# Kernel tuning notes

Measured on AMD Instinct MI355X. Metric: run time of the kernel, lower is better.

The kernel has to match this reference:

```python
import jax, jax.numpy as jnp
import numpy as np

N, K, D = 16384, 2048, 512

def setup_inputs() -> dict:
    key = jax.random.key(0)
    kx, kmu, kstd = jax.random.split(key, 3)
    x = jax.random.normal(kx, (N, D), dtype=jnp.float32)
    mu = jax.random.normal(kmu, (K, D), dtype=jnp.float32)
    std = jax.random.uniform(kstd, (K, D), dtype=jnp.float32)  # positive so log(sum(std)) is defined
    return {"x": x, "mu": mu, "std": std}

def reference(x, mu, std):
    x_sq = jnp.sum(x * x, axis=1)                      # [N]
    mu_sq = jnp.sum(mu * mu, axis=1)                   # [K]
    sqdist = x_sq[:, None] - 2.0 * (x @ mu.T) + mu_sq[None, :]  # [N, K]
    denom = 2.0 * jnp.sum(std * std, axis=1) + 1e-8    # [K]
    log_std_sum = jnp.log(jnp.sum(std, axis=1))        # [K]
    half_log_2pi = 0.5 * jnp.log(jnp.asarray(2.0 * np.pi, dtype=x.dtype))
    return -sqdist / denom[None, :] - log_std_sum[None, :] - half_log_2pi
```

## Files before the change

### kernel.cpp

```cpp
#include <hip/hip_runtime.h>
#include <hip/hip_bf16.h>
#include <stdint.h>

#define NN 16384
#define KK 2048
#define DD 512

typedef __bf16 bf16x8 __attribute__((ext_vector_type(8)));
typedef float f32x4 __attribute__((ext_vector_type(4)));
typedef unsigned short ushort_t;
typedef ushort_t us8 __attribute__((ext_vector_type(8)));

#define AS1(p) ((const __attribute__((address_space(1))) void*)(p))
#define AS3(p) ((__attribute__((address_space(3))) void*)(p))

__device__ inline ushort_t f2bf(float f) {
  uint32_t u = __float_as_uint(f);
  u += 0x7fffu + ((u >> 16) & 1u);
  return (ushort_t)(u >> 16);
}

__global__ __launch_bounds__(256) void prep_x(const float* __restrict__ x,
                                              ushort_t* __restrict__ xb,
                                              float* __restrict__ x_sq) {
  const int wave = threadIdx.x >> 6;
  const int lane = threadIdx.x & 63;
  const int row = blockIdx.x * 4 + wave;
  const float* xr = x + (size_t)row * DD + lane * 8;
  float4 v0 = *reinterpret_cast<const float4*>(xr);
  float4 v1 = *reinterpret_cast<const float4*>(xr + 4);
  float s = v0.x*v0.x + v0.y*v0.y + v0.z*v0.z + v0.w*v0.w
          + v1.x*v1.x + v1.y*v1.y + v1.z*v1.z + v1.w*v1.w;
  us8 o;
  o[0]=f2bf(v0.x); o[1]=f2bf(v0.y); o[2]=f2bf(v0.z); o[3]=f2bf(v0.w);
  o[4]=f2bf(v1.x); o[5]=f2bf(v1.y); o[6]=f2bf(v1.z); o[7]=f2bf(v1.w);
  *reinterpret_cast<us8*>(xb + (size_t)row * DD + lane * 8) = o;
  #pragma unroll
  for (int off = 32; off; off >>= 1) s += __shfl_xor(s, off, 64);
  if (lane == 0) x_sq[row] = s;
}

__global__ __launch_bounds__(256) void prep_mu(const float* __restrict__ mu,
                                               const float* __restrict__ sd,
                                               ushort_t* __restrict__ mub,
                                               float* __restrict__ inv_denom,
                                               float* __restrict__ beta) {
  const int wave = threadIdx.x >> 6;
  const int lane = threadIdx.x & 63;
  const int row = blockIdx.x * 4 + wave;
  const float* mr = mu + (size_t)row * DD + lane * 8;
  float4 v0 = *reinterpret_cast<const float4*>(mr);
  float4 v1 = *reinterpret_cast<const float4*>(mr + 4);
  float musq = v0.x*v0.x + v0.y*v0.y + v0.z*v0.z + v0.w*v0.w
             + v1.x*v1.x + v1.y*v1.y + v1.z*v1.z + v1.w*v1.w;
  us8 o;
  o[0]=f2bf(v0.x); o[1]=f2bf(v0.y); o[2]=f2bf(v0.z); o[3]=f2bf(v0.w);
  o[4]=f2bf(v1.x); o[5]=f2bf(v1.y); o[6]=f2bf(v1.z); o[7]=f2bf(v1.w);
  *reinterpret_cast<us8*>(mub + (size_t)row * DD + lane * 8) = o;

  const float* sr = sd + (size_t)row * DD + lane * 8;
  float4 s0 = *reinterpret_cast<const float4*>(sr);
  float4 s1 = *reinterpret_cast<const float4*>(sr + 4);
  float ssum = s0.x + s0.y + s0.z + s0.w + s1.x + s1.y + s1.z + s1.w;
  float ssq  = s0.x*s0.x + s0.y*s0.y + s0.z*s0.z + s0.w*s0.w
             + s1.x*s1.x + s1.y*s1.y + s1.z*s1.z + s1.w*s1.w;
  #pragma unroll
  for (int off = 32; off; off >>= 1) {
    musq += __shfl_xor(musq, off, 64);
    ssum += __shfl_xor(ssum, off, 64);
    ssq  += __shfl_xor(ssq,  off, 64);
  }
  if (lane == 0) {
    float idn = 1.0f / (2.0f * ssq + 1e-8f);
    inv_denom[row] = idn;
    beta[row] = musq * idn + logf(ssum) + 0.91893853320467274f;
  }
}

__global__ __launch_bounds__(256) void gemm_eval(const ushort_t* __restrict__ xb,
                                                 const ushort_t* __restrict__ mub,
                                                 const float* __restrict__ x_sq,
                                                 const float* __restrict__ inv_denom,
                                                 const float* __restrict__ beta,
                                                 float* __restrict__ out) {
  __shared__ __align__(16) ushort_t As[128 * 32];
  __shared__ __align__(16) ushort_t Bs[128 * 32];

  const int t = threadIdx.x;
  const int lane = t & 63;
  const int w = t >> 6;
  const int wrow = w >> 1;
  const int wcol = w & 1;

  const int bm = blockIdx.x >> 4;
  const int bn = blockIdx.x & 15;
  const int brow = bm * 128;
  const int bcol = bn * 128;

  f32x4 acc[4][4];
  #pragma unroll
  for (int m = 0; m < 4; ++m)
    #pragma unroll
    for (int c = 0; c < 4; ++c)
      acc[m][c] = (f32x4){0.f, 0.f, 0.f, 0.f};

  const int c0 = t;
  const int c1 = t + 256;

  const int rl = lane & 15;
  const int slot = lane >> 4;

  for (int kt = 0; kt < DD / 32; ++kt) {
    const int kb = kt * 32;
    {
      const ushort_t* g0 = xb + (size_t)(brow + (c0 >> 2)) * DD + kb + (c0 & 3) * 8;
      __builtin_amdgcn_global_load_lds(AS1(g0), AS3(As + c0 * 8), 16, 0, 0);
      const ushort_t* g1 = xb + (size_t)(brow + (c1 >> 2)) * DD + kb + (c1 & 3) * 8;
      __builtin_amdgcn_global_load_lds(AS1(g1), AS3(As + c1 * 8), 16, 0, 0);
      const ushort_t* h0 = mub + (size_t)(bcol + (c0 >> 2)) * DD + kb + (c0 & 3) * 8;
      __builtin_amdgcn_global_load_lds(AS1(h0), AS3(Bs + c0 * 8), 16, 0, 0);
      const ushort_t* h1 = mub + (size_t)(bcol + (c1 >> 2)) * DD + kb + (c1 & 3) * 8;
      __builtin_amdgcn_global_load_lds(AS1(h1), AS3(Bs + c1 * 8), 16, 0, 0);
    }
    __syncthreads();

    const bf16x8* A8 = reinterpret_cast<const bf16x8*>(As);
    const bf16x8* B8 = reinterpret_cast<const bf16x8*>(Bs);
    bf16x8 af[4], bfr[4];
    #pragma unroll
    for (int m = 0; m < 4; ++m)
      af[m] = A8[(wrow * 64 + m * 16 + rl) * 4 + slot];
    #pragma unroll
    for (int c = 0; c < 4; ++c)
      bfr[c] = B8[(wcol * 64 + c * 16 + rl) * 4 + slot];

    #pragma unroll
    for (int m = 0; m < 4; ++m)
      #pragma unroll
      for (int c = 0; c < 4; ++c)
        acc[m][c] = __builtin_amdgcn_mfma_f32_16x16x32_bf16(af[m], bfr[c], acc[m][c], 0, 0, 0);

    __syncthreads();
  }

  const int rh = lane >> 4;
  float inv[4], bet[4];
  #pragma unroll
  for (int c = 0; c < 4; ++c) {
    int k = bcol + wcol * 64 + c * 16 + rl;
    inv[c] = inv_denom[k];
    bet[c] = beta[k];
  }
  #pragma unroll
  for (int m = 0; m < 4; ++m) {
    #pragma unroll
    for (int r = 0; r < 4; ++r) {
      int n = brow + wrow * 64 + m * 16 + rh * 4 + r;
      float xs = x_sq[n];
      size_t base = (size_t)n * KK + bcol + wcol * 64;
      #pragma unroll
      for (int c = 0; c < 4; ++c) {
        out[base + c * 16 + rl] = (2.0f * acc[m][c][r] - xs) * inv[c] - bet[c];
      }
    }
  }
}

extern "C" void kernel_launch(void* const* d_in, const int* in_sizes, int n_in,
                              void* d_out, int out_size, void* d_ws, size_t ws_size,
                              hipStream_t stream) {
  const float* x   = (const float*)d_in[0];
  const float* mu  = (const float*)d_in[1];
  const float* sd  = (const float*)d_in[2];
  float* out = (float*)d_out;

  char* ws = (char*)d_ws;
  ushort_t* xb        = (ushort_t*)(ws);
  ushort_t* mub       = (ushort_t*)(ws + 16777216);
  float*    x_sq      = (float*)(ws + 18874368);
  float*    inv_denom = (float*)(ws + 18939904);
  float*    beta      = (float*)(ws + 18948096);

  prep_x<<<NN / 4, 256, 0, stream>>>(x, xb, x_sq);
  prep_mu<<<KK / 4, 256, 0, stream>>>(mu, sd, mub, inv_denom, beta);
  gemm_eval<<<(NN / 128) * (KK / 128), 256, 0, stream>>>(xb, mub, x_sq, inv_denom, beta, out);
}
```

Baseline: 202.3 us.

## Retile GEMM to 256x256 blocks with MFMA-ready layout and double-buffered LDS

The prep kernels now write the bf16 copies of x and mu in a pre-tiled, fragment-ordered layout, so each K-tile is one contiguous 32 KB chunk that can be copied straight into LDS and read with conflict-free per-lane loads. The GEMM grows to 256x256 tiles with 512 threads and 64-deep K steps. It double-buffers LDS so the next tile's global-to-LDS copy overlaps the MFMAs, and it adds block-index swizzling and s_setprio around the MFMA bursts. Together these aim to raise data reuse and cut both the LDS bank conflicts and the per-iteration barrier stalls. The cost is 128 KB of LDS per block, more accumulator registers, a fixed-shape layout, and hand-placed barriers and waitcnts that must stay correct.

```diff
diff --git a/kernel.cpp b/kernel.cpp
--- a/kernel.cpp
+++ b/kernel.cpp
@@ -14,11 +14,16 @@
 #define AS1(p) ((const __attribute__((address_space(1))) void*)(p))
 #define AS3(p) ((__attribute__((address_space(3))) void*)(p))
 
+#define FENCE() asm volatile("" ::: "memory")
+#define SBAR()  do { FENCE(); __builtin_amdgcn_s_barrier(); FENCE(); } while (0)
+#define WAITVM0() asm volatile("s_waitcnt vmcnt(0)" ::: "memory")
+
 __device__ inline ushort_t f2bf(float f) {
   uint32_t u = __float_as_uint(f);
   u += 0x7fffu + ((u >> 16) & 1u);
   return (ushort_t)(u >> 16);
 }
+
 
 __global__ __launch_bounds__(256) void prep_x(const float* __restrict__ x,
                                               ushort_t* __restrict__ xb,
@@ -34,9 +39,14 @@
   us8 o;
   o[0]=f2bf(v0.x); o[1]=f2bf(v0.y); o[2]=f2bf(v0.z); o[3]=f2bf(v0.w);
   o[4]=f2bf(v1.x); o[5]=f2bf(v1.y); o[6]=f2bf(v1.z); o[7]=f2bf(v1.w);
-  *reinterpret_cast<us8*>(xb + (size_t)row * DD + lane * 8) = o;
-  #pragma unroll
-  for (int off = 32; off; off >>= 1) s += __shfl_xor(s, off, 64);
+
+  const int br = row >> 8, m = (row >> 4) & 15, r = row & 15;
+  const int kt = lane >> 3, cc2 = lane & 7, ks = cc2 >> 2, slot = cc2 & 3;
+  size_t off = (size_t)(br * 8 + kt) * 16384 + (m * 2 + ks) * 512 + slot * 128 + r * 8;
+  *reinterpret_cast<us8*>(xb + off) = o;
+
+  #pragma unroll
+  for (int offs = 32; offs; offs >>= 1) s += __shfl_xor(s, offs, 64);
   if (lane == 0) x_sq[row] = s;
 }
 
@@ -56,7 +66,11 @@
   us8 o;
   o[0]=f2bf(v0.x); o[1]=f2bf(v0.y); o[2]=f2bf(v0.z); o[3]=f2bf(v0.w);
   o[4]=f2bf(v1.x); o[5]=f2bf(v1.y); o[6]=f2bf(v1.z); o[7]=f2bf(v1.w);
-  *reinterpret_cast<us8*>(mub + (size_t)row * DD + lane * 8) = o;
+
+  const int bc = row >> 8, cB = (row >> 4) & 15, r = row & 15;
+  const int kt = lane >> 3, cc2 = lane & 7, ks = cc2 >> 2, slot = cc2 & 3;
+  size_t off = (size_t)(bc * 8 + kt) * 16384 + (cB * 2 + ks) * 512 + slot * 128 + r * 8;
+  *reinterpret_cast<us8*>(mub + off) = o;
 
   const float* sr = sd + (size_t)row * DD + lane * 8;
   float4 s0 = *reinterpret_cast<const float4*>(sr);
@@ -65,10 +79,10 @@
   float ssq  = s0.x*s0.x + s0.y*s0.y + s0.z*s0.z + s0.w*s0.w
              + s1.x*s1.x + s1.y*s1.y + s1.z*s1.z + s1.w*s1.w;
   #pragma unroll
-  for (int off = 32; off; off >>= 1) {
-    musq += __shfl_xor(musq, off, 64);
-    ssum += __shfl_xor(ssum, off, 64);
-    ssq  += __shfl_xor(ssq,  off, 64);
+  for (int offs = 32; offs; offs >>= 1) {
+    musq += __shfl_xor(musq, offs, 64);
+    ssum += __shfl_xor(ssum, offs, 64);
+    ssq  += __shfl_xor(ssq,  offs, 64);
   }
   if (lane == 0) {
     float idn = 1.0f / (2.0f * ssq + 1e-8f);
@@ -77,93 +91,114 @@
   }
 }
 
-__global__ __launch_bounds__(256) void gemm_eval(const ushort_t* __restrict__ xb,
-                                                 const ushort_t* __restrict__ mub,
-                                                 const float* __restrict__ x_sq,
-                                                 const float* __restrict__ inv_denom,
-                                                 const float* __restrict__ beta,
-                                                 float* __restrict__ out) {
-  __shared__ __align__(16) ushort_t As[128 * 32];
-  __shared__ __align__(16) ushort_t Bs[128 * 32];
-
-  const int t = threadIdx.x;
-  const int lane = t & 63;
-  const int w = t >> 6;
-  const int wrow = w >> 1;
-  const int wcol = w & 1;
-
-  const int bm = blockIdx.x >> 4;
-  const int bn = blockIdx.x & 15;
-  const int brow = bm * 128;
-  const int bcol = bn * 128;
-
-  f32x4 acc[4][4];
-  #pragma unroll
-  for (int m = 0; m < 4; ++m)
+__global__ __launch_bounds__(512, 2) void gemm_eval(const ushort_t* __restrict__ xb,
+                                                    const ushort_t* __restrict__ mub,
+                                                    const float* __restrict__ x_sq,
+                                                    const float* __restrict__ inv_denom,
+                                                    const float* __restrict__ beta,
+                                                    float* __restrict__ out) {
+  __shared__ __align__(16) ushort_t As[2][16384];
+  __shared__ __align__(16) ushort_t Bs[2][16384];
+
+  const int t0 = threadIdx.x;
+  const int lane = t0 & 63;
+  const int w = t0 >> 6;
+  const int wrow = w >> 2;
+  const int wcol = w & 3;
+
+  const int bid = blockIdx.x;
+  const int swz = (bid & 7) * 64 + (bid >> 3);
+  const int bm = swz >> 3, bn = swz & 7;
+
+  const ushort_t* Ag = xb  + (size_t)bm * (8 * 16384);
+  const ushort_t* Bg = mub + (size_t)bn * (8 * 16384);
+
+  f32x4 acc[8][4];
+  #pragma unroll
+  for (int mmi = 0; mmi < 8; ++mmi)
     #pragma unroll
-    for (int c = 0; c < 4; ++c)
-      acc[m][c] = (f32x4){0.f, 0.f, 0.f, 0.f};
-
-  const int c0 = t;
-  const int c1 = t + 256;
-
-  const int rl = lane & 15;
-  const int slot = lane >> 4;
-
-  for (int kt = 0; kt < DD / 32; ++kt) {
-    const int kb = kt * 32;
-    {
-      const ushort_t* g0 = xb + (size_t)(brow + (c0 >> 2)) * DD + kb + (c0 & 3) * 8;
-      __builtin_amdgcn_global_load_lds(AS1(g0), AS3(As + c0 * 8), 16, 0, 0);
-      const ushort_t* g1 = xb + (size_t)(brow + (c1 >> 2)) * DD + kb + (c1 & 3) * 8;
-      __builtin_amdgcn_global_load_lds(AS1(g1), AS3(As + c1 * 8), 16, 0, 0);
-      const ushort_t* h0 = mub + (size_t)(bcol + (c0 >> 2)) * DD + kb + (c0 & 3) * 8;
-      __builtin_amdgcn_global_load_lds(AS1(h0), AS3(Bs + c0 * 8), 16, 0, 0);
-      const ushort_t* h1 = mub + (size_t)(bcol + (c1 >> 2)) * DD + kb + (c1 & 3) * 8;
-      __builtin_amdgcn_global_load_lds(AS1(h1), AS3(Bs + c1 * 8), 16, 0, 0);
+    for (int cc = 0; cc < 4; ++cc)
+      acc[mmi][cc] = (f32x4){0.f, 0.f, 0.f, 0.f};
+
+#define STAGE(kt, dbuf) do {                                                        \
+    const ushort_t* as_ = Ag + (size_t)(kt) * 16384;                                \
+    const ushort_t* bs_ = Bg + (size_t)(kt) * 16384;                                \
+    ushort_t* ad_ = &As[dbuf][0];                                                   \
+    ushort_t* bd_ = &Bs[dbuf][0];                                                   \
+    __builtin_amdgcn_global_load_lds(AS1(as_ + t0*8),        AS3(ad_ + t0*8),        16, 0, 0); \
+    __builtin_amdgcn_global_load_lds(AS1(as_ + (t0+512)*8),  AS3(ad_ + (t0+512)*8),  16, 0, 0); \
+    __builtin_amdgcn_global_load_lds(AS1(as_ + (t0+1024)*8), AS3(ad_ + (t0+1024)*8), 16, 0, 0); \
+    __builtin_amdgcn_global_load_lds(AS1(as_ + (t0+1536)*8), AS3(ad_ + (t0+1536)*8), 16, 0, 0); \
+    __builtin_amdgcn_global_load_lds(AS1(bs_ + t0*8),        AS3(bd_ + t0*8),        16, 0, 0); \
+    __builtin_amdgcn_global_load_lds(AS1(bs_ + (t0+512)*8),  AS3(bd_ + (t0+512)*8),  16, 0, 0); \
+    __builtin_amdgcn_global_load_lds(AS1(bs_ + (t0+1024)*8), AS3(bd_ + (t0+1024)*8), 16, 0, 0); \
+    __builtin_amdgcn_global_load_lds(AS1(bs_ + (t0+1536)*8), AS3(bd_ + (t0+1536)*8), 16, 0, 0); \
+  } while (0)
+
+  STAGE(0, 0);
+  WAITVM0();
+  SBAR();
+
+  for (int t = 0; t < 8; ++t) {
+    const ushort_t* Acur = &As[t & 1][0];
+    const ushort_t* Bcur = &Bs[t & 1][0];
+    bf16x8 bfrag[4][2];
+    #pragma unroll
+    for (int q = 0; q < 4; ++q) {
+      bf16x8 af[2][2];
+      #pragma unroll
+      for (int i = 0; i < 2; ++i)
+        #pragma unroll
+        for (int ks = 0; ks < 2; ++ks)
+          af[i][ks] = *reinterpret_cast<const bf16x8*>(
+              Acur + ((wrow * 8 + q * 2 + i) * 2 + ks) * 512 + lane * 8);
+      if (q == 0) {
+        #pragma unroll
+        for (int cc = 0; cc < 4; ++cc)
+          #pragma unroll
+          for (int ks = 0; ks < 2; ++ks)
+            bfrag[cc][ks] = *reinterpret_cast<const bf16x8*>(
+                Bcur + ((wcol * 4 + cc) * 2 + ks) * 512 + lane * 8);
+        if (t < 7) STAGE(t + 1, (t + 1) & 1);
+      }
+      SBAR();
+      __builtin_amdgcn_s_setprio(1);
+      #pragma unroll
+      for (int i = 0; i < 2; ++i)
+        #pragma unroll
+        for (int cc = 0; cc < 4; ++cc)
+          #pragma unroll
+          for (int ks = 0; ks < 2; ++ks)
+            acc[q * 2 + i][cc] = __builtin_amdgcn_mfma_f32_16x16x32_bf16(
+                af[i][ks], bfrag[cc][ks], acc[q * 2 + i][cc], 0, 0, 0);
+      __builtin_amdgcn_s_setprio(0);
+      if (q == 3) WAITVM0();
+      SBAR();
     }
-    __syncthreads();
-
-    const bf16x8* A8 = reinterpret_cast<const bf16x8*>(As);
-    const bf16x8* B8 = reinterpret_cast<const bf16x8*>(Bs);
-    bf16x8 af[4], bfr[4];
+  }
+
+  const int rl = lane & 15, rh = lane >> 4;
+  const int colbase = bn * 256 + wcol * 64;
+  float inv[4], bet[4];
+  #pragma unroll
+  for (int cc = 0; cc < 4; ++cc) {
+    inv[cc] = inv_denom[colbase + cc * 16 + rl];
+    bet[cc] = beta[colbase + cc * 16 + rl];
+  }
+  #pragma unroll
+  for (int mmi = 0; mmi < 8; ++mmi) {
+    const int nb = bm * 256 + wrow * 128 + mmi * 16 + rh * 4;
     #pragma unroll
-    for (int m = 0; m < 4; ++m)
-      af[m] = A8[(wrow * 64 + m * 16 + rl) * 4 + slot];
-    #pragma unroll
-    for (int c = 0; c < 4; ++c)
-      bfr[c] = B8[(wcol * 64 + c * 16 + rl) * 4 + slot];
-
-    #pragma unroll
-    for (int m = 0; m < 4; ++m)
+    for (int reg = 0; reg < 4; ++reg) {
+      const int n = nb + reg;
+      const float xs = x_sq[n];
+      float* op = out + (size_t)n * KK + colbase;
       #pragma unroll
-      for (int c = 0; c < 4; ++c)
-        acc[m][c] = __builtin_amdgcn_mfma_f32_16x16x32_bf16(af[m], bfr[c], acc[m][c], 0, 0, 0);
-
-    __syncthreads();
-  }
-
-  const int rh = lane >> 4;
-  float inv[4], bet[4];
-  #pragma unroll
-  for (int c = 0; c < 4; ++c) {
-    int k = bcol + wcol * 64 + c * 16 + rl;
-    inv[c] = inv_denom[k];
-    bet[c] = beta[k];
-  }
-  #pragma unroll
-  for (int m = 0; m < 4; ++m) {
-    #pragma unroll
-    for (int r = 0; r < 4; ++r) {
-      int n = brow + wrow * 64 + m * 16 + rh * 4 + r;
-      float xs = x_sq[n];
-      size_t base = (size_t)n * KK + bcol + wcol * 64;
-      #pragma unroll
-      for (int c = 0; c < 4; ++c) {
-        out[base + c * 16 + rl] = (2.0f * acc[m][c][r] - xs) * inv[c] - bet[c];
-      }
+      for (int cc = 0; cc < 4; ++cc)
+        op[cc * 16 + rl] = (2.0f * acc[mmi][cc][reg] - xs) * inv[cc] - bet[cc];
     }
   }
+#undef STAGE
 }
 
 extern "C" void kernel_launch(void* const* d_in, const int* in_sizes, int n_in,
@@ -183,5 +218,5 @@
 
   prep_x<<<NN / 4, 256, 0, stream>>>(x, xb, x_sq);
   prep_mu<<<KK / 4, 256, 0, stream>>>(mu, sd, mub, inv_denom, beta);
-  gemm_eval<<<(NN / 128) * (KK / 128), 256, 0, stream>>>(xb, mub, x_sq, inv_denom, beta, out);
-}
+  gemm_eval<<<(NN / 256) * (KK / 256), 512, 0, stream>>>(xb, mub, x_sq, inv_denom, beta, out);
+}
```

After: 202.2 us. About the same (-0.0%).
